# Optimization experiments

Measured on AMD Instinct MI355X. Metric: run time of the kernel, lower is better.

The kernel has to match this reference:

```python
import jax, jax.numpy as jnp
import numpy as np

HIDDEN = 256

def setup_inputs() -> dict:
    key = jax.random.key(0)
    ks = jax.random.split(key, 8)
    B, T, D, O, H = 128, 1024, 512, 128, HIDDEN
    s_ih = 1.0 / np.sqrt(H)
    inp = {
        "input_x": jax.random.normal(ks[0], (B, T, D), dtype=jnp.float32),
        # PyTorch LSTM params, gate order (i, f, g, o)
        "W_ih": jax.random.uniform(ks[1], (4 * H, D), minval=-s_ih, maxval=s_ih, dtype=jnp.float32),
        "W_hh": jax.random.uniform(ks[2], (4 * H, H), minval=-s_ih, maxval=s_ih, dtype=jnp.float32),
        "b_ih": jax.random.uniform(ks[3], (4 * H,), minval=-s_ih, maxval=s_ih, dtype=jnp.float32),
        "b_hh": jax.random.uniform(ks[4], (4 * H,), minval=-s_ih, maxval=s_ih, dtype=jnp.float32),
        "W_out": jax.random.uniform(ks[5], (O, H), minval=-s_ih, maxval=s_ih, dtype=jnp.float32),
        "b_out": jax.random.uniform(ks[6], (O,), minval=-s_ih, maxval=s_ih, dtype=jnp.float32),
    }
    return inp

def _lstm_last_hidden(input_x, W_ih, W_hh, b_ih, b_hh):
    B, T, D = input_x.shape
    H = HIDDEN
    # Batch the input projection over all timesteps (one big GEMM): [B,T,4H]
    xg = jnp.einsum("btd,gd->btg", input_x, W_ih) + b_ih + b_hh
    xg = jnp.transpose(xg, (1, 0, 2))  # [T,B,4H] for scan over time

    def step(carry, xg_t):
        h, c = carry
        gates = xg_t + h @ W_hh.T  # [B,4H]
        i, f, g, o = jnp.split(gates, 4, axis=-1)
        i = jax.nn.sigmoid(i)
        f = jax.nn.sigmoid(f)
        g = jnp.tanh(g)
        o = jax.nn.sigmoid(o)
        c = f * c + i * g
        h = o * jnp.tanh(c)
        return (h, c), None

    h0 = jnp.zeros((B, H), dtype=input_x.dtype)
    c0 = jnp.zeros((B, H), dtype=input_x.dtype)
    (h_T, _), _ = jax.lax.scan(step, (h0, c0), xg)
    return h_T  # == y[:, -1, :]

def reference(input_x, W_ih, W_hh, b_ih, b_hh, W_out, b_out):
    h_T = _lstm_last_hidden(input_x, W_ih, W_hh, b_ih, b_hh)
    # Dropout is identity in eval mode; squeeze(dim=1) is a no-op for O>1.
    return h_T @ W_out.T + b_out  # [B, O]
```

## Files before the change

### kernel.cpp

```cpp
#include <hip/hip_runtime.h>
#include <hip/hip_bf16.h>

#define B_ 128
#define T_ 1024
#define D_ 512
#define H_ 256
#define G_ 1024

typedef __bf16 bf16_t;
typedef __bf16 bf16x8 __attribute__((ext_vector_type(8)));
typedef __bf16 bf16x4 __attribute__((ext_vector_type(4)));
typedef float  f32x4  __attribute__((ext_vector_type(4)));

__device__ __forceinline__ float fast_rcp(float x) { return __builtin_amdgcn_rcpf(x); }

__device__ __forceinline__ float sigmoid_f(float x) {
  return fast_rcp(1.0f + __expf(-x));
}
__device__ __forceinline__ float tanh_f(float x) {
  x = fminf(fmaxf(x, -15.0f), 15.0f);
  float e = __expf(-2.0f * x);
  return (1.0f - e) * fast_rcp(1.0f + e);
}

__device__ __forceinline__ void barrier_lds_only() {
  asm volatile("s_waitcnt lgkmcnt(0)\n\ts_barrier" ::: "memory");
}

__device__ __forceinline__ void gload_lds16(const void* g, void* l) {
  __builtin_amdgcn_global_load_lds(
      (const __attribute__((address_space(1))) void*)g,
      (__attribute__((address_space(3))) void*)l, 16, 0, 0);
}

__global__ __launch_bounds__(256) void prep_kernel(
    const float* __restrict__ Whh, const float* __restrict__ bih,
    const float* __restrict__ bhh, bf16_t* __restrict__ whhb,
    float* __restrict__ bias) {
  int i = blockIdx.x * 256 + threadIdx.x;
  if (i < G_ * H_) whhb[i] = (bf16_t)Whh[i];
  if (i < G_) bias[i] = bih[i] + bhh[i];
}

__global__ __launch_bounds__(256) void prep_full_kernel(
    const float* __restrict__ Whh, const float* __restrict__ bih,
    const float* __restrict__ bhh, const float* __restrict__ Wih,
    bf16_t* __restrict__ whhb, bf16_t* __restrict__ wihb,
    float* __restrict__ bias) {
  int i = blockIdx.x * 256 + threadIdx.x;
  if (i < G_ * H_) whhb[i] = (bf16_t)Whh[i];
  wihb[i] = (bf16_t)Wih[i];
  if (i < G_) bias[i] = bih[i] + bhh[i];
}

__global__ __launch_bounds__(256) void xconv_kernel(
    const float* __restrict__ X, bf16_t* __restrict__ Xb) {
  const int n4 = (B_ * T_ * D_) / 4;
  const int stride = gridDim.x * 256;
  for (int i = blockIdx.x * 256 + threadIdx.x; i < n4; i += stride) {
    float4 v = ((const float4*)X)[i];
    ((bf16x4*)Xb)[i] =
        (bf16x4){(bf16_t)v.x, (bf16_t)v.y, (bf16_t)v.z, (bf16_t)v.w};
  }
}

__global__ __launch_bounds__(512) void xg_gemm_fast(
    const bf16_t* __restrict__ Xb, const bf16_t* __restrict__ Wihb,
    const float* __restrict__ bias, bf16_t* __restrict__ xg2) {
  __shared__ __align__(16) bf16_t As[128][64];
  __shared__ __align__(16) bf16_t Bs[256][64];

  const int tid = threadIdx.x;
  const int lane = tid & 63;
  const int w = tid >> 6;
  const int wm = w >> 2;
  const int wn = w & 3;
  const int q = lane >> 4;
  const int l15 = lane & 15;
  const int m0 = blockIdx.x * 128;
  const int ch0 = blockIdx.y * 64;

  const int lr = lane >> 3;
  const int ls = (lane & 7) ^ (lr & 7);
  const int lc = ls * 8;

  f32x4 acc[4][4];
  #pragma unroll
  for (int mi = 0; mi < 4; ++mi)
    #pragma unroll
    for (int nf = 0; nf < 4; ++nf) acc[mi][nf] = (f32x4){0.f, 0.f, 0.f, 0.f};

  const char* As0 = (const char*)&As[0][0];
  const char* Bs0 = (const char*)&Bs[0][0];

  for (int kt = 0; kt < 8; ++kt) {
    const int k0 = kt * 64;
    __syncthreads();
    #pragma unroll
    for (int j = 0; j < 2; ++j) {
      const int c = w * 2 + j;
      gload_lds16(Xb + (size_t)(m0 + c * 8 + lr) * D_ + k0 + lc,
                  (char*)&As[0][0] + c * 1024);
    }
    #pragma unroll
    for (int j = 0; j < 4; ++j) {
      const int c = w * 4 + j;
      const int br = c * 8 + lr;
      const int wr = (br >> 6) * 256 + ch0 + (br & 63);
      gload_lds16(Wihb + (size_t)wr * D_ + k0 + lc,
                  (char*)&Bs[0][0] + c * 1024);
    }
    __syncthreads();
    #pragma unroll
    for (int kk = 0; kk < 2; ++kk) {
      bf16x8 a[4], b[4];
      #pragma unroll
      for (int mi = 0; mi < 4; ++mi) {
        const int row = wm * 64 + mi * 16 + l15;
        a[mi] = *(const bf16x8*)(As0 + row * 128 +
                                 (((kk * 4 + q) ^ (row & 7)) * 16));
      }
      #pragma unroll
      for (int nf = 0; nf < 4; ++nf) {
        const int row = nf * 64 + wn * 16 + l15;
        b[nf] = *(const bf16x8*)(Bs0 + row * 128 +
                                 (((kk * 4 + q) ^ (row & 7)) * 16));
      }
      #pragma unroll
      for (int mi = 0; mi < 4; ++mi)
        #pragma unroll
        for (int nf = 0; nf < 4; ++nf)
          acc[mi][nf] =
              __builtin_amdgcn_mfma_f32_16x16x32_bf16(a[mi], b[nf], acc[mi][nf], 0, 0, 0);
    }
  }
  const int cc = ch0 + wn * 16 + l15;
  const float bv0 = bias[cc], bv1 = bias[256 + cc];
  const float bv2 = bias[512 + cc], bv3 = bias[768 + cc];
  #pragma unroll
  for (int mi = 0; mi < 4; ++mi) {
    #pragma unroll
    for (int i = 0; i < 4; ++i) {
      const int row = m0 + wm * 64 + mi * 16 + 4 * q + i;
      bf16x4 v = (bf16x4){(bf16_t)(acc[mi][0][i] + bv0), (bf16_t)(acc[mi][1][i] + bv1),
                          (bf16_t)(acc[mi][2][i] + bv2), (bf16_t)(acc[mi][3][i] + bv3)};
      *(bf16x4*)(xg2 + ((size_t)row * 256 + cc) * 4) = v;
    }
  }
}

__global__ __launch_bounds__(512) void xg_gemm(
    const float* __restrict__ X, const float* __restrict__ Wih,
    const float* __restrict__ bias, bf16_t* __restrict__ xg2) {
  __shared__ __align__(16) bf16_t As[128][72];
  __shared__ __align__(16) bf16_t Bs[256][72];

  const int tid = threadIdx.x;
  const int lane = tid & 63;
  const int w = tid >> 6;
  const int q = lane >> 4;
  const int l15 = lane & 15;
  const int m0 = blockIdx.x * 128;
  const int ch0 = blockIdx.y * 64;

  f32x4 acc[16];
  #pragma unroll
  for (int n = 0; n < 16; ++n) acc[n] = (f32x4){0.f, 0.f, 0.f, 0.f};

  for (int kt = 0; kt < 8; ++kt) {
    const int k0 = kt * 64;
    __syncthreads();
    #pragma unroll
    for (int i = 0; i < 4; ++i) {
      int f = tid + 512 * i;
      int r = f >> 4, c4 = f & 15;
      float4 va = *(const float4*)(X + (size_t)(m0 + r) * D_ + k0 + c4 * 4);
      *(bf16x4*)&As[r][c4 * 4] =
          (bf16x4){(bf16_t)va.x, (bf16_t)va.y, (bf16_t)va.z, (bf16_t)va.w};
    }
    #pragma unroll
    for (int j = 0; j < 8; ++j) {
      int f = tid + 512 * j;
      int r = f >> 4, c4 = f & 15;
      int wr = (r >> 6) * 256 + ch0 + (r & 63);
      float4 vb = *(const float4*)(Wih + (size_t)wr * D_ + k0 + c4 * 4);
      *(bf16x4*)&Bs[r][c4 * 4] =
          (bf16x4){(bf16_t)vb.x, (bf16_t)vb.y, (bf16_t)vb.z, (bf16_t)vb.w};
    }
    __syncthreads();
    #pragma unroll
    for (int kk = 0; kk < 2; ++kk) {
      bf16x8 a = *(const bf16x8*)&As[16 * w + l15][kk * 32 + q * 8];
      #pragma unroll
      for (int n = 0; n < 16; ++n) {
        bf16x8 b = *(const bf16x8*)&Bs[16 * n + l15][kk * 32 + q * 8];
        acc[n] = __builtin_amdgcn_mfma_f32_16x16x32_bf16(a, b, acc[n], 0, 0, 0);
      }
    }
  }
  #pragma unroll
  for (int cs = 0; cs < 4; ++cs) {
    const int cc = ch0 + cs * 16 + l15;
    float bv0 = bias[cc], bv1 = bias[256 + cc];
    float bv2 = bias[512 + cc], bv3 = bias[768 + cc];
    #pragma unroll
    for (int i = 0; i < 4; ++i) {
      int row = m0 + 16 * w + 4 * q + i;
      bf16x4 v = (bf16x4){(bf16_t)(acc[cs][i] + bv0), (bf16_t)(acc[4 + cs][i] + bv1),
                          (bf16_t)(acc[8 + cs][i] + bv2), (bf16_t)(acc[12 + cs][i] + bv3)};
      *(bf16x4*)(xg2 + ((size_t)row * 256 + cc) * 4) = v;
    }
  }
}

__global__ __launch_bounds__(512, 2) void lstm_scan(
    const bf16_t* __restrict__ xg2, const bf16_t* __restrict__ Whh,
    float* __restrict__ hT) {
  __shared__ __align__(16) bf16_t wlds[8 * 16 * 512];
  __shared__ __align__(16) bf16_t hbuf[2][16][264];

  const int tid = threadIdx.x;
  const int lane = tid & 63;
  const int w = tid >> 6;
  const int q = lane >> 4;
  const int l15 = lane & 15;
  const int b0 = blockIdx.x * 8;
  const int rq = (q & 1) * 4 + (q >> 1) * 2;
  const bool hi = (lane >= 32);

  bf16x8 wreg[6][8];
  #pragma unroll
  for (int p2 = 0; p2 < 2; ++p2) {
    #pragma unroll
    for (int g2 = 0; g2 < 4; ++g2) {
      const int j = p2 * 4 + g2;
      const bf16_t* src =
          Whh + (size_t)(g2 * 256 + 32 * w + 16 * p2 + l15) * H_ + q * 8;
      #pragma unroll
      for (int kk = 0; kk < 8; ++kk) {
        bf16x8 v = *(const bf16x8*)(src + kk * 32);
        if (j < 6) {
          wreg[j][kk] = v;
        } else {
          *(bf16x8*)&wlds[(size_t)((w * 16 + (g2 - 2) * 8 + kk)) * 512 + lane * 8] = v;
        }
      }
    }
  }

  for (int i = tid; i < 2 * 16 * 264; i += 512) ((bf16_t*)hbuf)[i] = (bf16_t)0.0f;
  __syncthreads();

  float cst[2][2];
  #pragma unroll
  for (int p = 0; p < 2; ++p) { cst[p][0] = 0.f; cst[p][1] = 0.f; }

  const bf16_t* xp[2][2];
  #pragma unroll
  for (int p = 0; p < 2; ++p)
    #pragma unroll
    for (int k = 0; k < 2; ++k)
      xp[p][k] = xg2 + (size_t)(b0 + rq + k) * (size_t)T_ * 1024 + (32 * w + 16 * p + l15) * 4;

  bf16x4 xv[2][2], xn[2][2];
  #pragma unroll
  for (int p = 0; p < 2; ++p)
    #pragma unroll
    for (int k = 0; k < 2; ++k) {
      xv[p][k] = *(const bf16x4*)xp[p][k];
      xp[p][k] += 1024;
    }

  auto step = [&](int t, bf16x4 (&xc)[2][2], bf16x4 (&xf)[2][2]) {
    #pragma unroll
    for (int p = 0; p < 2; ++p)
      #pragma unroll
      for (int k = 0; k < 2; ++k) {
        xf[p][k] = *(const bf16x4*)xp[p][k];
        xp[p][k] += 1024;
      }
    const int cur = t & 1;
    #pragma unroll
    for (int p = 0; p < 2; ++p) {
      f32x4 acc[4];
      #pragma unroll
      for (int g = 0; g < 4; ++g) acc[g] = (f32x4){0.f, 0.f, 0.f, 0.f};
      #pragma unroll
      for (int kk = 0; kk < 8; ++kk) {
        bf16x8 a = *(const bf16x8*)&hbuf[cur][l15][kk * 32 + q * 8];
        if (p == 0) {
          acc[0] = __builtin_amdgcn_mfma_f32_16x16x32_bf16(a, wreg[0][kk], acc[0], 0, 0, 0);
          acc[1] = __builtin_amdgcn_mfma_f32_16x16x32_bf16(a, wreg[1][kk], acc[1], 0, 0, 0);
          acc[2] = __builtin_amdgcn_mfma_f32_16x16x32_bf16(a, wreg[2][kk], acc[2], 0, 0, 0);
          acc[3] = __builtin_amdgcn_mfma_f32_16x16x32_bf16(a, wreg[3][kk], acc[3], 0, 0, 0);
        } else {
          acc[0] = __builtin_amdgcn_mfma_f32_16x16x32_bf16(a, wreg[4][kk], acc[0], 0, 0, 0);
          acc[1] = __builtin_amdgcn_mfma_f32_16x16x32_bf16(a, wreg[5][kk], acc[1], 0, 0, 0);
          bf16x8 bg = *(const bf16x8*)&wlds[(size_t)(w * 16 + kk) * 512 + lane * 8];
          bf16x8 bo = *(const bf16x8*)&wlds[(size_t)(w * 16 + 8 + kk) * 512 + lane * 8];
          acc[2] = __builtin_amdgcn_mfma_f32_16x16x32_bf16(a, bg, acc[2], 0, 0, 0);
          acc[3] = __builtin_amdgcn_mfma_f32_16x16x32_bf16(a, bo, acc[3], 0, 0, 0);
        }
      }
      float G0[4], G1[4];
      #pragma unroll
      for (int g = 0; g < 4; ++g) {
        float s2 = __shfl(acc[g][2], lane ^ 32, 64);
        float s3 = __shfl(acc[g][3], lane ^ 32, 64);
        G0[g] = hi ? s2 : acc[g][0];
        G1[g] = hi ? s3 : acc[g][1];
      }
      const int c = 32 * w + 16 * p + l15;
      #pragma unroll
      for (int k = 0; k < 2; ++k) {
        const float* Gv_ = k ? G1 : G0;
        float gi = Gv_[0] + (float)xc[p][k][0];
        float gf = Gv_[1] + (float)xc[p][k][1];
        float gg = Gv_[2] + (float)xc[p][k][2];
        float go = Gv_[3] + (float)xc[p][k][3];
        float I = sigmoid_f(gi);
        float F = sigmoid_f(gf);
        float Gg = tanh_f(gg);
        float Ov = sigmoid_f(go);
        float cv = F * cst[p][k] + I * Gg;
        cst[p][k] = cv;
        float hv = Ov * tanh_f(cv);
        hbuf[cur ^ 1][rq + k][c] = (bf16_t)hv;
        if (t == T_ - 1) hT[(size_t)(b0 + rq + k) * H_ + c] = hv;
      }
    }
    barrier_lds_only();
  };

  #pragma unroll 1
  for (int t = 0; t < T_; t += 2) {
    step(t, xv, xn);
    step(t + 1, xn, xv);
  }
}

__global__ __launch_bounds__(128) void head_gemm(
    const float* __restrict__ hT, const float* __restrict__ Wout,
    const float* __restrict__ bout, float* __restrict__ out) {
  __shared__ float hrow[H_];
  const int b = blockIdx.x;
  const int o = threadIdx.x;
  hrow[o] = hT[(size_t)b * H_ + o];
  hrow[o + 128] = hT[(size_t)b * H_ + 128 + o];
  __syncthreads();
  float s = bout[o];
  const float* wr = Wout + (size_t)o * H_;
  #pragma unroll 8
  for (int j = 0; j < H_; ++j) s += hrow[j] * wr[j];
  out[(size_t)b * 128 + o] = s;
}

extern "C" void kernel_launch(void* const* d_in, const int* in_sizes, int n_in,
                              void* d_out, int out_size, void* d_ws, size_t ws_size,
                              hipStream_t stream) {
  const float* X    = (const float*)d_in[0];
  const float* Wih  = (const float*)d_in[1];
  const float* Whh  = (const float*)d_in[2];
  const float* bih  = (const float*)d_in[3];
  const float* bhh  = (const float*)d_in[4];
  const float* Wout = (const float*)d_in[5];
  const float* bout = (const float*)d_in[6];
  float* out = (float*)d_out;

  char* ws = (char*)d_ws;
  const size_t XG_BYTES   = (size_t)B_ * T_ * G_ * 2;
  const size_t WHHB_BYTES = (size_t)G_ * H_ * 2;
  const size_t BIAS_BYTES = (size_t)G_ * 4;
  const size_t HT_BYTES   = (size_t)B_ * H_ * 4;
  const size_t WIHB_BYTES = (size_t)G_ * D_ * 2;
  const size_t XB_BYTES   = (size_t)B_ * T_ * D_ * 2;
  bf16_t* xg2  = (bf16_t*)ws;
  bf16_t* whhb = (bf16_t*)(ws + XG_BYTES);
  float*  bias = (float*)(ws + XG_BYTES + WHHB_BYTES);
  float*  hT   = (float*)(ws + XG_BYTES + WHHB_BYTES + BIAS_BYTES);
  bf16_t* wihb = (bf16_t*)(ws + XG_BYTES + WHHB_BYTES + BIAS_BYTES + HT_BYTES);
  bf16_t* xb   = (bf16_t*)(ws + XG_BYTES + WHHB_BYTES + BIAS_BYTES + HT_BYTES + WIHB_BYTES);

  const size_t NEED_FAST =
      XG_BYTES + WHHB_BYTES + BIAS_BYTES + HT_BYTES + WIHB_BYTES + XB_BYTES;

  if (ws_size >= NEED_FAST) {
    prep_full_kernel<<<dim3(2048), 256, 0, stream>>>(Whh, bih, bhh, Wih, whhb, wihb, bias);
    xconv_kernel<<<dim3(4096), 256, 0, stream>>>(X, xb);
    xg_gemm_fast<<<dim3((B_ * T_) / 128, 4), 512, 0, stream>>>(xb, wihb, bias, xg2);
  } else {
    prep_kernel<<<dim3(1024), 256, 0, stream>>>(Whh, bih, bhh, whhb, bias);
    xg_gemm<<<dim3((B_ * T_) / 128, 4), 512, 0, stream>>>(X, Wih, bias, xg2);
  }
  lstm_scan<<<dim3(B_ / 8), 512, 0, stream>>>(xg2, whhb, hT);
  head_gemm<<<dim3(B_), 128, 0, stream>>>(hT, Wout, bout, out);
}
```

Baseline: 3.110 ms.

## Keep recurrent weights in registers with 1024-thread LSTM scan blocks

```diff
diff --git a/kernel.cpp b/kernel.cpp
--- a/kernel.cpp
+++ b/kernel.cpp
@@ -210,6 +210,93 @@
                           (bf16_t)(acc[8 + cs][i] + bv2), (bf16_t)(acc[12 + cs][i] + bv3)};
       *(bf16x4*)(xg2 + ((size_t)row * 256 + cc) * 4) = v;
     }
+  }
+}
+
+__global__ __launch_bounds__(1024) void lstm_scan16(
+    const bf16_t* __restrict__ xg2, const bf16_t* __restrict__ whhb,
+    float* __restrict__ hT) {
+  __shared__ __align__(16) bf16_t hbuf[2][16][264];
+
+  const int tid = threadIdx.x;
+  const int lane = tid & 63;
+  const int w = tid >> 6;
+  const int q = lane >> 4;
+  const int l15 = lane & 15;
+  const int b0 = blockIdx.x * 8;
+  const int ch = 16 * w + l15;
+  const int rq = (q & 1) * 4 + (q >> 1) * 2;
+  const bool hi = (lane >= 32);
+
+  bf16x8 wf[4][8];
+  #pragma unroll
+  for (int g = 0; g < 4; ++g)
+    #pragma unroll
+    for (int kk = 0; kk < 8; ++kk)
+      wf[g][kk] = *(const bf16x8*)(whhb + ((size_t)g * 256 + ch) * 256 + kk * 32 + q * 8);
+
+  for (int i = tid; i < 2 * 16 * 264; i += 1024) ((bf16_t*)hbuf)[i] = (bf16_t)0.0f;
+  __syncthreads();
+
+  float cst0 = 0.f, cst1 = 0.f;
+
+  const bf16_t* xp0 = xg2 + (size_t)(b0 + rq) * T_ * 1024 + ch * 4;
+  const bf16_t* xp1 = xg2 + (size_t)(b0 + rq + 1) * T_ * 1024 + ch * 4;
+  bf16x4 xv0 = *(const bf16x4*)xp0, xv1 = *(const bf16x4*)xp1;
+  xp0 += 1024; xp1 += 1024;
+
+  #pragma unroll 1
+  for (int t = 0; t < T_; ++t) {
+    bf16x4 xn0 = *(const bf16x4*)xp0;
+    bf16x4 xn1 = *(const bf16x4*)xp1;
+    xp0 += 1024; xp1 += 1024;
+    const int cur = t & 1;
+
+    f32x4 acc[4];
+    #pragma unroll
+    for (int g = 0; g < 4; ++g) acc[g] = (f32x4){0.f, 0.f, 0.f, 0.f};
+    #pragma unroll
+    for (int kk = 0; kk < 8; ++kk) {
+      bf16x8 a = *(const bf16x8*)&hbuf[cur][l15][kk * 32 + q * 8];
+      acc[0] = __builtin_amdgcn_mfma_f32_16x16x32_bf16(a, wf[0][kk], acc[0], 0, 0, 0);
+      acc[1] = __builtin_amdgcn_mfma_f32_16x16x32_bf16(a, wf[1][kk], acc[1], 0, 0, 0);
+      acc[2] = __builtin_amdgcn_mfma_f32_16x16x32_bf16(a, wf[2][kk], acc[2], 0, 0, 0);
+      acc[3] = __builtin_amdgcn_mfma_f32_16x16x32_bf16(a, wf[3][kk], acc[3], 0, 0, 0);
+    }
+
+    float G0[4], G1[4];
+    #pragma unroll
+    for (int g = 0; g < 4; ++g) {
+      float s2 = __shfl(acc[g][2], lane ^ 32, 64);
+      float s3 = __shfl(acc[g][3], lane ^ 32, 64);
+      G0[g] = hi ? s2 : acc[g][0];
+      G1[g] = hi ? s3 : acc[g][1];
+    }
+
+    float gi0 = G0[0] + (float)xv0[0], gf0 = G0[1] + (float)xv0[1];
+    float gg0 = G0[2] + (float)xv0[2], go0 = G0[3] + (float)xv0[3];
+    float I0 = sigmoid_f(gi0), F0 = sigmoid_f(gf0);
+    float Gg0 = tanh_f(gg0), O0 = sigmoid_f(go0);
+    float cv0 = F0 * cst0 + I0 * Gg0; cst0 = cv0;
+    float hv0 = O0 * tanh_f(cv0);
+
+    float gi1 = G1[0] + (float)xv1[0], gf1 = G1[1] + (float)xv1[1];
+    float gg1 = G1[2] + (float)xv1[2], go1 = G1[3] + (float)xv1[3];
+    float I1 = sigmoid_f(gi1), F1 = sigmoid_f(gf1);
+    float Gg1 = tanh_f(gg1), O1 = sigmoid_f(go1);
+    float cv1 = F1 * cst1 + I1 * Gg1; cst1 = cv1;
+    float hv1 = O1 * tanh_f(cv1);
+
+    hbuf[cur ^ 1][rq][ch]     = (bf16_t)hv0;
+    hbuf[cur ^ 1][rq + 1][ch] = (bf16_t)hv1;
+
+    if (t == T_ - 1) {
+      hT[(size_t)(b0 + rq) * H_ + ch]     = hv0;
+      hT[(size_t)(b0 + rq + 1) * H_ + ch] = hv1;
+    }
+
+    xv0 = xn0; xv1 = xn1;
+    barrier_lds_only();
   }
 }
 
@@ -388,10 +475,11 @@
     prep_full_kernel<<<dim3(2048), 256, 0, stream>>>(Whh, bih, bhh, Wih, whhb, wihb, bias);
     xconv_kernel<<<dim3(4096), 256, 0, stream>>>(X, xb);
     xg_gemm_fast<<<dim3((B_ * T_) / 128, 4), 512, 0, stream>>>(xb, wihb, bias, xg2);
+    lstm_scan16<<<dim3(B_ / 8), 1024, 0, stream>>>(xg2, whhb, hT);
   } else {
     prep_kernel<<<dim3(1024), 256, 0, stream>>>(Whh, bih, bhh, whhb, bias);
     xg_gemm<<<dim3((B_ * T_) / 128, 4), 512, 0, stream>>>(X, Wih, bias, xg2);
-  }
-  lstm_scan<<<dim3(B_ / 8), 512, 0, stream>>>(xg2, whhb, hT);
+    lstm_scan<<<dim3(B_ / 8), 512, 0, stream>>>(xg2, whhb, hT);
+  }
   head_gemm<<<dim3(B_), 128, 0, stream>>>(hT, Wout, bout, out);
 }
```

After: 5.996 ms. 1.93x slower.
